# Optimization experiments

Measured on AMD Instinct MI355X. Metric: run time of the kernel, lower is better.

The kernel has to match this reference:

```python
import jax, jax.numpy as jnp
import numpy as np

N_NODES = 50000
N_EDGES = 800000
D_IN = 128
D_OUT = 128
N_GRAPHS = 512
N_CONVS = 5
EPS = 1e-5


def setup_inputs() -> dict:
    key = jax.random.key(0)
    ks = jax.random.split(key, 8)
    x = jax.random.normal(ks[0], (N_NODES, D_IN), dtype=jnp.float32)
    edge_index = jax.random.randint(ks[1], (2, N_EDGES), 0, N_NODES, dtype=jnp.int32)
    batch = jnp.sort(jax.random.randint(ks[2], (N_NODES,), 0, N_GRAPHS, dtype=jnp.int32))
    s = 1.0 / np.sqrt(D_IN)
    W_rel = jax.random.normal(ks[3], (N_CONVS, D_OUT, D_IN), dtype=jnp.float32) * s
    b_rel = jax.random.normal(ks[4], (N_CONVS, D_OUT), dtype=jnp.float32) * s
    W_root = jax.random.normal(ks[5], (N_CONVS, D_OUT, D_IN), dtype=jnp.float32) * s
    gamma = jnp.ones((D_OUT,), dtype=jnp.float32)
    beta = jnp.zeros((D_OUT,), dtype=jnp.float32)
    Wc = jax.random.normal(ks[6], (96, D_OUT), dtype=jnp.float32) * (1.0 / np.sqrt(D_OUT))
    bc = jax.random.normal(ks[7], (96,), dtype=jnp.float32) * (1.0 / np.sqrt(D_OUT))
    return {"x": x, "edge_index": edge_index, "batch": batch, "i": 0,
            "W_rel": W_rel, "b_rel": b_rel, "W_root": W_root,
            "gamma": gamma, "beta": beta, "Wc": Wc, "bc": bc}


def reference(x, edge_index, batch, i, W_rel, b_rel, W_root, gamma, beta, Wc, bc):
    # --- 5 GraphConv branches, summed. GraphConv: lin_rel(sum_{j->i} x_j) + lin_root(x).
    # Sum over the 5 convs commutes with the linears, so fold the weights first.
    src, dst = edge_index[0], edge_index[1]
    agg = jax.ops.segment_sum(x[src], dst, num_segments=N_NODES)  # [N, D_in]
    Wr = jnp.sum(W_rel, axis=0)   # [D_out, D_in]
    Wt = jnp.sum(W_root, axis=0)  # [D_out, D_in]
    br = jnp.sum(b_rel, axis=0)   # [D_out]
    h = agg @ Wr.T + x @ Wt.T + br  # [N, D_out]
    # --- NodeLevelBatchNorm (training: batch stats over all nodes, biased var)
    mean = jnp.mean(h, axis=0)
    var = jnp.mean((h - mean) ** 2, axis=0)
    h = gamma * (h - mean) * jax.lax.rsqrt(var + EPS) + beta
    # --- global max pool over graphs, relu, classifier (i=0 -> no-dropout branch)
    pooled = jax.ops.segment_max(h, batch, num_segments=N_GRAPHS)  # [G, D_out]
    pooled = jax.nn.relu(pooled)
    return pooled @ Wc.T + bc  # [G, 96]
```

## Files before the change

kernel.cpp:

```cpp
#include <hip/hip_runtime.h>

#define EPS 1e-5f

constexpr int NN = 50000, NE = 800000, DD = 128, NG = 512, NC = 5, NO = 96;
constexpr int MAXB = 8192;
constexpr int NBUCK = 196;

typedef __attribute__((ext_vector_type(8))) short bf16x8;
typedef __attribute__((ext_vector_type(4))) float f32x4;

constexpr size_t HB   = 0;
constexpr size_t XB   = (size_t)NN * DD / 2;
constexpr size_t WB   = XB + (size_t)NN * DD / 2;
constexpr size_t BRO  = WB + DD * 256 / 2;
constexpr size_t CSUM = BRO + DD;
constexpr size_t CSQ  = CSUM + DD;
constexpr size_t POOL = CSQ + DD;
constexpr size_t GCNT = POOL + (size_t)NG * DD;
constexpr size_t ZEND = GCNT + 256;
constexpr size_t ROFF = ZEND;
constexpr size_t BSTOR= ROFF + NN + 1;
constexpr size_t CSR16= BSTOR + (size_t)NBUCK*MAXB;

constexpr int XCAST_B = NN * DD / 4 / 256;
constexpr int FOLD_B  = DD * DD / 256;
constexpr int BUCK_B  = (NE + 4095) / 4096;

static __device__ __forceinline__ unsigned short f2b(float f) {
    unsigned int u = __float_as_uint(f);
    return (unsigned short)((u + 0x7FFFu + ((u >> 16) & 1u)) >> 16);
}
static __device__ __forceinline__ float b2f(unsigned short h) {
    return __uint_as_float(((unsigned int)h) << 16);
}
static __device__ __forceinline__ unsigned fkey(float f) {
    unsigned u = __float_as_uint(f);
    return (u >> 31) ? ~u : (u | 0x80000000u);
}
static __device__ __forceinline__ float unfkey(unsigned k) {
    unsigned u = (k & 0x80000000u) ? (k ^ 0x80000000u) : ~k;
    return __uint_as_float(u);
}

__global__ __launch_bounds__(256) void k_prep(const float* __restrict__ x,
                                              const float* __restrict__ Wrel,
                                              const float* __restrict__ brel,
                                              const float* __restrict__ Wroot,
                                              const int* __restrict__ ei,
                                              float* __restrict__ ws, int* __restrict__ wi) {
    __shared__ int lcnt[256];
    __shared__ int lbase[256];
    int b = blockIdx.x, t = threadIdx.x;
    if (b < XCAST_B) {
        int i = b * 256 + t;
        float4 v = ((const float4*)x)[i];
        ushort4 o = {f2b(v.x), f2b(v.y), f2b(v.z), f2b(v.w)};
        ((ushort4*)(ws + XB))[i] = o;
    } else if (b < XCAST_B + FOLD_B) {
        int idx = (b - XCAST_B) * 256 + t;
        int k = idx >> 7, o = idx & 127;
        float wr = 0.f, wt = 0.f;
        for (int c = 0; c < NC; ++c) {
            wr += Wrel [c*DD*DD + o*DD + k];
            wt += Wroot[c*DD*DD + o*DD + k];
        }
        unsigned short* wb = (unsigned short*)(ws + WB);
        wb[o*256 + k]       = f2b(wr);
        wb[o*256 + 128 + k] = f2b(wt);
        if (k == 0) {
            float bias = 0.f;
            for (int c = 0; c < NC; ++c) bias += brel[c*DD + o];
            ws[BRO + o] = bias;
        }
    } else {
        int bb = b - XCAST_B - FOLD_B;
        lcnt[t] = 0;
        __syncthreads();
        int val[16], krk[16];
        #pragma unroll
        for (int j = 0; j < 16; ++j) {
            int e = bb * 4096 + j * 256 + t;
            krk[j] = -1;
            if (e < NE) {
                int d = ei[NE + e], s = ei[e];
                int key = d >> 8;
                int r = atomicAdd(&lcnt[key], 1);
                val[j] = s | ((d & 255) << 16);
                krk[j] = (key << 16) | r;
            }
        }
        __syncthreads();
        if (t < NBUCK && lcnt[t] > 0)
            lbase[t] = atomicAdd(&wi[GCNT + t], lcnt[t]);
        __syncthreads();
        #pragma unroll
        for (int j = 0; j < 16; ++j) {
            if (krk[j] >= 0) {
                int key = krk[j] >> 16, r = krk[j] & 0xFFFF;
                int p = lbase[key] + r;
                if (p < MAXB) wi[BSTOR + (size_t)key * MAXB + p] = val[j];
            }
        }
    }
}

__global__ __launch_bounds__(256) void k_sort(int* __restrict__ wi) {
    __shared__ int eds[MAXB];
    __shared__ unsigned short srt[MAXB];
    __shared__ int cnt[256], cnt2[256], lscan[256], gall[256];
    int t = threadIdx.x, b = blockIdx.x;
    int g = wi[GCNT + t];
    gall[t] = g; lscan[t] = g; cnt[t] = 0;
    __syncthreads();
    for (int off = 1; off < 256; off <<= 1) {
        int u = (t >= off) ? gall[t - off] : 0;
        __syncthreads();
        gall[t] += u;
        __syncthreads();
    }
    int base = gall[b] - lscan[b];
    int C = lscan[b]; if (C > MAXB) C = MAXB;
    __syncthreads();
    for (int i = t; i < C; i += 256) {
        int v = wi[BSTOR + (size_t)b * MAXB + i];
        eds[i] = v;
        atomicAdd(&cnt[v >> 16], 1);
    }
    __syncthreads();
    int cv = cnt[t];
    for (int off = 1; off < 256; off <<= 1) {
        int u = (t >= off) ? cnt[t - off] : 0;
        __syncthreads();
        cnt[t] += u;
        __syncthreads();
    }
    lscan[t] = cnt[t] - cv;
    cnt2[t] = 0;
    __syncthreads();
    int n = b * 256 + t;
    if (n < NN) wi[ROFF + n] = base + lscan[t];
    if (b == 0 && t == 0) wi[ROFF + NN] = NE;
    for (int i = t; i < C; i += 256) {
        int v = eds[i], k = v >> 16;
        int p = lscan[k] + atomicAdd(&cnt2[k], 1);
        srt[p] = (unsigned short)(v & 0xFFFF);
    }
    __syncthreads();
    unsigned short* csr = (unsigned short*)(wi + CSR16);
    for (int i = t; i < C; i += 256)
        csr[base + i] = srt[i];
}

__global__ __launch_bounds__(256) void k_gather(const int* __restrict__ wi,
                                                float* __restrict__ ws) {
    const unsigned short* xb = (const unsigned short*)(ws + XB);
    const unsigned short* csr = (const unsigned short*)(wi + CSR16);
    unsigned short* hb = (unsigned short*)(ws + HB);
    int tid = threadIdx.x;
    int n   = blockIdx.x * 16 + (tid >> 4);
    int sub = tid & 15;
    int c8  = sub * 8;
    if (n >= NN) return;
    int e0 = wi[ROFF + n], e1 = wi[ROFF + n + 1];
    int cnt = e1 - e0;
    float acc[8] = {};
    int base = 0;
    for (; base + 16 <= cnt; base += 16) {
        int myE = (int)csr[e0 + base + sub];
        #pragma unroll
        for (int j = 0; j < 16; ++j) {
            int s = __shfl(myE, j, 16);
            bf16x8 v = *(const bf16x8*)&xb[(size_t)s * DD + c8];
            #pragma unroll
            for (int c = 0; c < 8; ++c) acc[c] += b2f((unsigned short)v[c]);
        }
    }
    int rem = cnt - base;
    if (rem > 0) {
        int myE = (sub < rem) ? (int)csr[e0 + base + sub] : 0;
        for (int j = 0; j < rem; ++j) {
            int s = __shfl(myE, j, 16);
            bf16x8 v = *(const bf16x8*)&xb[(size_t)s * DD + c8];
            #pragma unroll
            for (int c = 0; c < 8; ++c) acc[c] += b2f((unsigned short)v[c]);
        }
    }
    bf16x8 o;
    #pragma unroll
    for (int c = 0; c < 8; ++c) o[c] = (short)f2b(acc[c]);
    *(bf16x8*)&hb[(size_t)n * DD + c8] = o;
}

__global__ __launch_bounds__(256) void k_gemm(const int* __restrict__ batch,
                                              float* __restrict__ ws) {
    __shared__ float sSum[128], sSq[128];
    __shared__ int batchS[128];
    __shared__ unsigned maxS[32][128];
    const unsigned short* hb = (const unsigned short*)(ws + HB);
    const unsigned short* xb = (const unsigned short*)(ws + XB);
    const unsigned short* wb = (const unsigned short*)(ws + WB);
    unsigned* poolU = (unsigned*)(ws + POOL);
    int tid  = threadIdx.x;
    if (tid < 128) { sSum[tid] = 0.f; sSq[tid] = 0.f; }
    for (int i = tid; i < 32 * 128; i += 256) ((unsigned*)maxS)[i] = 0u;
    if (tid < 128) {
        int r = blockIdx.x * 128 + tid; if (r > NN - 1) r = NN - 1;
        batchS[tid] = batch[r];
    }
    __syncthreads();
    int gBase = batchS[0];
    int wave = tid >> 6, lane = tid & 63;
    int ch = wave & 1, rg = wave >> 1;
    int quad = lane >> 4, l16 = lane & 15;
    bf16x8 bf[4][8];
    #pragma unroll
    for (int nt = 0; nt < 4; ++nt)
        #pragma unroll
        for (int kt = 0; kt < 8; ++kt)
            bf[nt][kt] = *(const bf16x8*)(wb + (size_t)(ch*64 + nt*16 + l16)*256 + kt*32 + quad*8);
    float bias[4], csum[4] = {}, csq[4] = {};
    #pragma unroll
    for (int nt = 0; nt < 4; ++nt) bias[nt] = ws[BRO + ch*64 + nt*16 + l16];
    #pragma unroll
    for (int c = 0; c < 4; ++c) {
        int lbase = rg * 64 + c * 16;
        int row0 = blockIdx.x * 128 + lbase;
        int arow = row0 + l16; if (arow > NN - 1) arow = NN - 1;
        const unsigned short* aggRow = hb + (size_t)arow * DD;
        const unsigned short* xRow   = xb + (size_t)arow * DD;
        bf16x8 af[8];
        #pragma unroll
        for (int kt = 0; kt < 8; ++kt)
            af[kt] = *(const bf16x8*)((kt < 4 ? aggRow + kt*32 : xRow + kt*32 - 128) + quad*8);
        f32x4 acc[4] = {};
        #pragma unroll
        for (int kt = 0; kt < 8; ++kt)
            #pragma unroll
            for (int nt = 0; nt < 4; ++nt)
                acc[nt] = __builtin_amdgcn_mfma_f32_16x16x32_bf16(af[kt], bf[nt][kt], acc[nt], 0, 0, 0);
        #pragma unroll
        for (int nt = 0; nt < 4; ++nt) {
            int col = ch*64 + nt*16 + l16;
            float mx = 0.f; int gcur = -1;
            #pragma unroll
            for (int r = 0; r < 4; ++r) {
                int row = row0 + quad*4 + r;
                if (row < NN) {
                    float v = acc[nt][r] + bias[nt];
                    csum[nt] += v; csq[nt] += v * v;
                    int g = batchS[lbase + quad*4 + r];
                    if (g != gcur) {
                        if (gcur >= 0) {
                            int rel = gcur - gBase;
                            if (rel < 32) atomicMax(&maxS[rel][col], fkey(mx));
                            else atomicMax(&poolU[(size_t)gcur * DD + col], fkey(mx));
                        }
                        gcur = g; mx = v;
                    } else mx = fmaxf(mx, v);
                }
            }
            if (gcur >= 0) {
                int rel = gcur - gBase;
                if (rel < 32) atomicMax(&maxS[rel][col], fkey(mx));
                else atomicMax(&poolU[(size_t)gcur * DD + col], fkey(mx));
            }
        }
    }
    __syncthreads();
    int span = batchS[127] - gBase + 1; if (span > 32) span = 32;
    for (int i = tid; i < span * 128; i += 256) {
        unsigned k = maxS[i >> 7][i & 127];
        if (k) atomicMax(&poolU[(size_t)(gBase + (i >> 7)) * DD + (i & 127)], k);
    }
    #pragma unroll
    for (int nt = 0; nt < 4; ++nt) {
        int col = ch*64 + nt*16 + l16;
        float cs = csum[nt], cq = csq[nt];
        cs += __shfl_xor(cs, 16); cs += __shfl_xor(cs, 32);
        cq += __shfl_xor(cq, 16); cq += __shfl_xor(cq, 32);
        if (quad == 0) { atomicAdd(&sSum[col], cs); atomicAdd(&sSq[col], cq); }
    }
    __syncthreads();
    if (tid < 128) {
        atomicAdd(&ws[CSUM + tid], sSum[tid]);
        atomicAdd(&ws[CSQ  + tid], sSq[tid]);
    }
}

__global__ __launch_bounds__(128) void k_out(const float* __restrict__ gamma,
                                             const float* __restrict__ beta,
                                             const float* __restrict__ Wc,
                                             const float* __restrict__ bc,
                                             const float* __restrict__ ws,
                                             float* __restrict__ out) {
    __shared__ float pS[128];
    int g = blockIdx.x, t = threadIdx.x;
    float mean = ws[CSUM + t] * (1.0f / NN);
    float var  = ws[CSQ + t] * (1.0f / NN) - mean * mean;
    float sc   = gamma[t] * rsqrtf(var + EPS);
    float sh   = beta[t] - sc * mean;
    unsigned k = ((const unsigned*)(ws + POOL))[(size_t)g * DD + t];
    float p = 0.f;
    if (k) p = fmaxf(unfkey(k) * sc + sh, 0.f);
    pS[t] = p;
    __syncthreads();
    if (t < NO) {
        float acc = bc[t];
        #pragma unroll 8
        for (int kk = 0; kk < DD; ++kk) acc += pS[kk] * Wc[t*DD + kk];
        out[g*NO + t] = acc;
    }
}

extern "C" void kernel_launch(void* const* d_in, const int* in_sizes, int n_in,
                              void* d_out, int out_size, void* d_ws, size_t ws_size,
                              hipStream_t stream) {
    const float* x     = (const float*)d_in[0];
    const int*   ei    = (const int*)  d_in[1];
    const int*   batch = (const int*)  d_in[2];
    const float* Wrel  = (const float*)d_in[4];
    const float* brel  = (const float*)d_in[5];
    const float* Wroot = (const float*)d_in[6];
    const float* gamma = (const float*)d_in[7];
    const float* beta  = (const float*)d_in[8];
    const float* Wc    = (const float*)d_in[9];
    const float* bc    = (const float*)d_in[10];
    float* ws  = (float*)d_ws;
    int*   wi  = (int*)d_ws;
    float* out = (float*)d_out;

    hipMemsetAsync(ws + CSUM, 0, (ZEND - CSUM) * sizeof(float), stream);

    k_prep  <<<XCAST_B + FOLD_B + BUCK_B, 256, 0, stream>>>(x, Wrel, brel, Wroot, ei, ws, wi);
    k_sort  <<<NBUCK, 256, 0, stream>>>(wi);
    k_gather<<<(NN + 15)/16, 256, 0, stream>>>(wi, ws);
    k_gemm  <<<(NN + 127)/128, 256, 0, stream>>>(batch, ws);
    k_out   <<<NG, 128, 0, stream>>>(gamma, beta, Wc, bc, ws, out);
}
```

Measured before the change: 188.1 us.

## Fuse neighbor gather with GEMM, keeping aggregated rows in shared memory

```diff
diff --git a/kernel.cpp b/kernel.cpp
--- a/kernel.cpp
+++ b/kernel.cpp
@@ -151,139 +151,148 @@
         csr[base + i] = srt[i];
 }
 
-__global__ __launch_bounds__(256) void k_gather(const int* __restrict__ wi,
-                                                float* __restrict__ ws) {
-    const unsigned short* xb = (const unsigned short*)(ws + XB);
+__global__ __launch_bounds__(256) void k_gg(const int* __restrict__ batch,
+                                            const int* __restrict__ wi,
+                                            float* __restrict__ ws) {
+    __shared__ __align__(16) unsigned short aggS[32 * 128];
+    __shared__ int batchS[32];
+    __shared__ unsigned maxS[4][128];
+    const unsigned short* xb  = (const unsigned short*)(ws + XB);
+    const unsigned short* wbp = (const unsigned short*)(ws + WB);
     const unsigned short* csr = (const unsigned short*)(wi + CSR16);
-    unsigned short* hb = (unsigned short*)(ws + HB);
+    unsigned* poolU = (unsigned*)(ws + POOL);
     int tid = threadIdx.x;
-    int n   = blockIdx.x * 16 + (tid >> 4);
-    int sub = tid & 15;
-    int c8  = sub * 8;
-    if (n >= NN) return;
-    int e0 = wi[ROFF + n], e1 = wi[ROFF + n + 1];
-    int cnt = e1 - e0;
-    float acc[8] = {};
-    int base = 0;
-    for (; base + 16 <= cnt; base += 16) {
-        int myE = (int)csr[e0 + base + sub];
-        #pragma unroll
-        for (int j = 0; j < 16; ++j) {
-            int s = __shfl(myE, j, 16);
-            bf16x8 v = *(const bf16x8*)&xb[(size_t)s * DD + c8];
-            #pragma unroll
-            for (int c = 0; c < 8; ++c) acc[c] += b2f((unsigned short)v[c]);
-        }
-    }
-    int rem = cnt - base;
-    if (rem > 0) {
-        int myE = (sub < rem) ? (int)csr[e0 + base + sub] : 0;
-        for (int j = 0; j < rem; ++j) {
-            int s = __shfl(myE, j, 16);
-            bf16x8 v = *(const bf16x8*)&xb[(size_t)s * DD + c8];
-            #pragma unroll
-            for (int c = 0; c < 8; ++c) acc[c] += b2f((unsigned short)v[c]);
-        }
-    }
-    bf16x8 o;
-    #pragma unroll
-    for (int c = 0; c < 8; ++c) o[c] = (short)f2b(acc[c]);
-    *(bf16x8*)&hb[(size_t)n * DD + c8] = o;
-}
-
-__global__ __launch_bounds__(256) void k_gemm(const int* __restrict__ batch,
-                                              float* __restrict__ ws) {
-    __shared__ float sSum[128], sSq[128];
-    __shared__ int batchS[128];
-    __shared__ unsigned maxS[32][128];
-    const unsigned short* hb = (const unsigned short*)(ws + HB);
-    const unsigned short* xb = (const unsigned short*)(ws + XB);
-    const unsigned short* wb = (const unsigned short*)(ws + WB);
-    unsigned* poolU = (unsigned*)(ws + POOL);
-    int tid  = threadIdx.x;
-    if (tid < 128) { sSum[tid] = 0.f; sSq[tid] = 0.f; }
-    for (int i = tid; i < 32 * 128; i += 256) ((unsigned*)maxS)[i] = 0u;
-    if (tid < 128) {
-        int r = blockIdx.x * 128 + tid; if (r > NN - 1) r = NN - 1;
+    int row0g = blockIdx.x * 32;
+
+    for (int i = tid; i < 4 * 128; i += 256) ((unsigned*)maxS)[i] = 0u;
+    if (tid < 32) {
+        int r = row0g + tid; if (r > NN - 1) r = NN - 1;
         batchS[tid] = batch[r];
     }
-    __syncthreads();
-    int gBase = batchS[0];
-    int wave = tid >> 6, lane = tid & 63;
-    int ch = wave & 1, rg = wave >> 1;
-    int quad = lane >> 4, l16 = lane & 15;
-    bf16x8 bf[4][8];
-    #pragma unroll
-    for (int nt = 0; nt < 4; ++nt)
-        #pragma unroll
-        for (int kt = 0; kt < 8; ++kt)
-            bf[nt][kt] = *(const bf16x8*)(wb + (size_t)(ch*64 + nt*16 + l16)*256 + kt*32 + quad*8);
-    float bias[4], csum[4] = {}, csq[4] = {};
-    #pragma unroll
-    for (int nt = 0; nt < 4; ++nt) bias[nt] = ws[BRO + ch*64 + nt*16 + l16];
-    #pragma unroll
-    for (int c = 0; c < 4; ++c) {
-        int lbase = rg * 64 + c * 16;
-        int row0 = blockIdx.x * 128 + lbase;
-        int arow = row0 + l16; if (arow > NN - 1) arow = NN - 1;
-        const unsigned short* aggRow = hb + (size_t)arow * DD;
-        const unsigned short* xRow   = xb + (size_t)arow * DD;
-        bf16x8 af[8];
-        #pragma unroll
-        for (int kt = 0; kt < 8; ++kt)
-            af[kt] = *(const bf16x8*)((kt < 4 ? aggRow + kt*32 : xRow + kt*32 - 128) + quad*8);
-        f32x4 acc[4] = {};
-        #pragma unroll
-        for (int kt = 0; kt < 8; ++kt)
-            #pragma unroll
-            for (int nt = 0; nt < 4; ++nt)
-                acc[nt] = __builtin_amdgcn_mfma_f32_16x16x32_bf16(af[kt], bf[nt][kt], acc[nt], 0, 0, 0);
-        #pragma unroll
-        for (int nt = 0; nt < 4; ++nt) {
-            int col = ch*64 + nt*16 + l16;
-            float mx = 0.f; int gcur = -1;
-            #pragma unroll
-            for (int r = 0; r < 4; ++r) {
-                int row = row0 + quad*4 + r;
-                if (row < NN) {
-                    float v = acc[nt][r] + bias[nt];
-                    csum[nt] += v; csq[nt] += v * v;
-                    int g = batchS[lbase + quad*4 + r];
-                    if (g != gcur) {
-                        if (gcur >= 0) {
-                            int rel = gcur - gBase;
-                            if (rel < 32) atomicMax(&maxS[rel][col], fkey(mx));
-                            else atomicMax(&poolU[(size_t)gcur * DD + col], fkey(mx));
-                        }
-                        gcur = g; mx = v;
-                    } else mx = fmaxf(mx, v);
+
+    {
+        int sub = tid & 15, c8 = sub * 8;
+        for (int round = 0; round < 2; ++round) {
+            int row = round * 16 + (tid >> 4);
+            int n = row0g + row;
+            float acc[8] = {};
+            if (n < NN) {
+                int e0 = wi[ROFF + n], e1 = wi[ROFF + n + 1];
+                int cnt = e1 - e0;
+                int base = 0;
+                for (; base + 16 <= cnt; base += 16) {
+                    int myE = (int)csr[e0 + base + sub];
+                    #pragma unroll
+                    for (int j = 0; j < 16; ++j) {
+                        int s = __shfl(myE, j, 16);
+                        bf16x8 v = *(const bf16x8*)&xb[(size_t)s * DD + c8];
+                        #pragma unroll
+                        for (int c = 0; c < 8; ++c) acc[c] += b2f((unsigned short)v[c]);
+                    }
+                }
+                int rem = cnt - base;
+                if (rem > 0) {
+                    int myE = (sub < rem) ? (int)csr[e0 + base + sub] : 0;
+                    for (int j = 0; j < rem; ++j) {
+                        int s = __shfl(myE, j, 16);
+                        bf16x8 v = *(const bf16x8*)&xb[(size_t)s * DD + c8];
+                        #pragma unroll
+                        for (int c = 0; c < 8; ++c) acc[c] += b2f((unsigned short)v[c]);
+                    }
                 }
             }
-            if (gcur >= 0) {
-                int rel = gcur - gBase;
-                if (rel < 32) atomicMax(&maxS[rel][col], fkey(mx));
-                else atomicMax(&poolU[(size_t)gcur * DD + col], fkey(mx));
+            bf16x8 o;
+            #pragma unroll
+            for (int c = 0; c < 8; ++c) o[c] = (short)f2b(acc[c]);
+            *(bf16x8*)((char*)aggS + row * 256 + ((sub * 16) ^ ((row & 7) << 4))) = o;
+        }
+    }
+    __syncthreads();
+
+    int wave = tid >> 6, lane = tid & 63;
+    int quad = lane >> 4, l16 = lane & 15;
+    int cw = wave * 32;
+    int gBase = batchS[0];
+    float bias[2] = { ws[BRO + cw + l16], ws[BRO + cw + 16 + l16] };
+    f32x4 acc[2][2] = {};
+    #pragma unroll
+    for (int rt = 0; rt < 2; ++rt) {
+        int row = rt * 16 + l16;
+        int arow = row0g + row; if (arow > NN - 1) arow = NN - 1;
+        const unsigned short* xRow = xb + (size_t)arow * DD;
+        bf16x8 af[8];
+        #pragma unroll
+        for (int kt = 0; kt < 4; ++kt)
+            af[kt] = *(const bf16x8*)((const char*)aggS + row * 256 +
+                                      ((kt * 64 + quad * 16) ^ ((row & 7) << 4)));
+        #pragma unroll
+        for (int kt = 4; kt < 8; ++kt)
+            af[kt] = *(const bf16x8*)(xRow + (kt - 4) * 32 + quad * 8);
+        #pragma unroll
+        for (int kt = 0; kt < 8; ++kt) {
+            bf16x8 b0 = *(const bf16x8*)(wbp + (size_t)(cw + l16) * 256 + kt * 32 + quad * 8);
+            bf16x8 b1 = *(const bf16x8*)(wbp + (size_t)(cw + 16 + l16) * 256 + kt * 32 + quad * 8);
+            acc[rt][0] = __builtin_amdgcn_mfma_f32_16x16x32_bf16(af[kt], b0, acc[rt][0], 0, 0, 0);
+            acc[rt][1] = __builtin_amdgcn_mfma_f32_16x16x32_bf16(af[kt], b1, acc[rt][1], 0, 0, 0);
+        }
+    }
+    float csum[2] = {}, csq[2] = {};
+    float mx[2]; int gcur = -1;
+    #pragma unroll
+    for (int rt = 0; rt < 2; ++rt) {
+        #pragma unroll
+        for (int r = 0; r < 4; ++r) {
+            int lrow = rt * 16 + quad * 4 + r;
+            int grow = row0g + lrow;
+            if (grow < NN) {
+                float v0 = acc[rt][0][r] + bias[0];
+                float v1 = acc[rt][1][r] + bias[1];
+                csum[0] += v0; csq[0] += v0 * v0;
+                csum[1] += v1; csq[1] += v1 * v1;
+                int g = batchS[lrow];
+                if (g != gcur) {
+                    if (gcur >= 0) {
+                        int rel = gcur - gBase;
+                        if (rel < 4) {
+                            atomicMax(&maxS[rel][cw + l16], fkey(mx[0]));
+                            atomicMax(&maxS[rel][cw + 16 + l16], fkey(mx[1]));
+                        } else {
+                            atomicMax(&poolU[(size_t)gcur * DD + cw + l16], fkey(mx[0]));
+                            atomicMax(&poolU[(size_t)gcur * DD + cw + 16 + l16], fkey(mx[1]));
+                        }
+                    }
+                    gcur = g; mx[0] = v0; mx[1] = v1;
+                } else {
+                    mx[0] = fmaxf(mx[0], v0); mx[1] = fmaxf(mx[1], v1);
+                }
             }
         }
     }
-    __syncthreads();
-    int span = batchS[127] - gBase + 1; if (span > 32) span = 32;
-    for (int i = tid; i < span * 128; i += 256) {
-        unsigned k = maxS[i >> 7][i & 127];
-        if (k) atomicMax(&poolU[(size_t)(gBase + (i >> 7)) * DD + (i & 127)], k);
+    if (gcur >= 0) {
+        int rel = gcur - gBase;
+        if (rel < 4) {
+            atomicMax(&maxS[rel][cw + l16], fkey(mx[0]));
+            atomicMax(&maxS[rel][cw + 16 + l16], fkey(mx[1]));
+        } else {
+            atomicMax(&poolU[(size_t)gcur * DD + cw + l16], fkey(mx[0]));
+            atomicMax(&poolU[(size_t)gcur * DD + cw + 16 + l16], fkey(mx[1]));
+        }
     }
     #pragma unroll
-    for (int nt = 0; nt < 4; ++nt) {
-        int col = ch*64 + nt*16 + l16;
-        float cs = csum[nt], cq = csq[nt];
+    for (int ct = 0; ct < 2; ++ct) {
+        float cs = csum[ct], cq = csq[ct];
         cs += __shfl_xor(cs, 16); cs += __shfl_xor(cs, 32);
         cq += __shfl_xor(cq, 16); cq += __shfl_xor(cq, 32);
-        if (quad == 0) { atomicAdd(&sSum[col], cs); atomicAdd(&sSq[col], cq); }
-    }
-    __syncthreads();
-    if (tid < 128) {
-        atomicAdd(&ws[CSUM + tid], sSum[tid]);
-        atomicAdd(&ws[CSQ  + tid], sSq[tid]);
+        if (quad == 0) {
+            atomicAdd(&ws[CSUM + cw + ct * 16 + l16], cs);
+            atomicAdd(&ws[CSQ  + cw + ct * 16 + l16], cq);
+        }
+    }
+    __syncthreads();
+    int span = batchS[31] - gBase + 1; if (span > 4) span = 4;
+    for (int i = tid; i < span * 128; i += 256) {
+        unsigned k = ((unsigned*)maxS)[i];
+        if (k) atomicMax(&poolU[(size_t)(gBase + (i >> 7)) * DD + (i & 127)], k);
     }
 }
 
@@ -331,9 +340,8 @@
 
     hipMemsetAsync(ws + CSUM, 0, (ZEND - CSUM) * sizeof(float), stream);
 
-    k_prep  <<<XCAST_B + FOLD_B + BUCK_B, 256, 0, stream>>>(x, Wrel, brel, Wroot, ei, ws, wi);
-    k_sort  <<<NBUCK, 256, 0, stream>>>(wi);
-    k_gather<<<(NN + 15)/16, 256, 0, stream>>>(wi, ws);
-    k_gemm  <<<(NN + 127)/128, 256, 0, stream>>>(batch, ws);
-    k_out   <<<NG, 128, 0, stream>>>(gamma, beta, Wc, bc, ws, out);
-}
+    k_prep <<<XCAST_B + FOLD_B + BUCK_B, 256, 0, stream>>>(x, Wrel, brel, Wroot, ei, ws, wi);
+    k_sort <<<NBUCK, 256, 0, stream>>>(wi);
+    k_gg   <<<(NN + 31)/32, 256, 0, stream>>>(batch, wi, ws);
+    k_out  <<<NG, 128, 0, stream>>>(gamma, beta, Wc, bc, ws, out);
+}
```

Result: slower. 201.8 us (+7.3%).
